# Performance work log

Hardware: AMD Instinct MI355X
Metric: run time of the kernel (lower is better)

The kernel has to match this reference:

```python
import jax, jax.numpy as jnp
import numpy as np

NUM_WORDS = 32768
MAX_CHARS = 20
NUM_CHARS = 128
EMB = 64
H = 128   # word_hidden_size (per direction)
C = 128   # context_vector_size


def setup_inputs() -> dict:
    key = jax.random.key(0)
    ks = jax.random.split(key, 16)
    s = 1.0 / np.sqrt(H)  # torch GRU default init scale
    u = lambda k, shape, sc: jax.random.uniform(k, shape, jnp.float32, -sc, sc)
    inp = {
        'padded_char_tensor': jax.random.randint(ks[0], (NUM_WORDS, MAX_CHARS), 0, NUM_CHARS),
        'sequence_lens': jax.random.randint(ks[1], (NUM_WORDS,), 1, MAX_CHARS + 1),
        'emb': jax.random.normal(ks[2], (NUM_CHARS, EMB), jnp.float32),
        # forward-direction GRU params (torch layout: gates r,z,n stacked)
        'Wih_f': u(ks[3], (3 * H, EMB), s),
        'Whh_f': u(ks[4], (3 * H, H), s),
        'bih_f': u(ks[5], (3 * H,), s),
        'bhh_f': u(ks[6], (3 * H,), s),
        # backward-direction GRU params
        'Wih_b': u(ks[7], (3 * H, EMB), s),
        'Whh_b': u(ks[8], (3 * H, H), s),
        'bih_b': u(ks[9], (3 * H,), s),
        'bhh_b': u(ks[10], (3 * H,), s),
        # word_projection Linear(2H -> C)
        'Wp': u(ks[11], (C, 2 * H), 1.0 / np.sqrt(2 * H)),
        'bp': u(ks[12], (C,), 1.0 / np.sqrt(2 * H)),
        # word context vector [C, 1]
        'ctx': u(ks[13], (C, 1), 0.1),
    }
    return inp


def _gru_dir(x_proj, Whh, bhh):
    # x_proj: [B, T, 3H] precomputed input projection; scan over T
    Hn = Whh.shape[1]
    def step(h, xt):
        hp = h @ Whh.T + bhh
        r = jax.nn.sigmoid(xt[:, :Hn] + hp[:, :Hn])
        z = jax.nn.sigmoid(xt[:, Hn:2 * Hn] + hp[:, Hn:2 * Hn])
        n = jnp.tanh(xt[:, 2 * Hn:] + r * hp[:, 2 * Hn:])
        h = (1.0 - z) * n + z * h
        return h, h
    h0 = jnp.zeros((x_proj.shape[0], Hn), x_proj.dtype)
    _, ys = jax.lax.scan(step, h0, x_proj.transpose(1, 0, 2))
    return ys.transpose(1, 0, 2)  # [B, T, H]


def _rev_within(x, lens):
    # reverse each sequence within its valid length (packed-sequence semantics)
    T = x.shape[1]
    t = jnp.arange(T)[None, :]
    idx = jnp.where(t < lens[:, None], lens[:, None] - 1 - t, t)
    return jnp.take_along_axis(x, idx[:, :, None], axis=1)


def _forward(chars, lens, emb, Wih_f, Whh_f, bih_f, bhh_f,
             Wih_b, Whh_b, bih_b, bhh_b, Wp, bp, ctx):
    x = emb[chars]  # [B, T, EMB]; dropout_p=0 -> identity
    mask = (jnp.arange(x.shape[1])[None, :] < lens[:, None])  # [B, T]
    out_f = _gru_dir(x @ Wih_f.T + bih_f, Whh_f, bhh_f)
    xb = _rev_within(x, lens)
    out_b = _gru_dir(xb @ Wih_b.T + bih_b, Whh_b, bhh_b)
    out_b = _rev_within(out_b, lens)
    # pad_packed_sequence zero-pads beyond each length
    out = jnp.concatenate([out_f, out_b], axis=-1) * mask[:, :, None]  # [B, T, 2H]
    proj = jnp.tanh(out @ Wp.T + bp)                # [B, T, C]
    scores = jnp.einsum('btc,c->bt', proj, ctx[:, 0])
    att = jax.nn.softmax(scores, axis=-1)           # softmax over char positions
    return jnp.einsum('bt,btd->bd', att, out)       # [B, 2H]


def reference(padded_char_tensor, sequence_lens, emb, Wih_f, Whh_f, bih_f, bhh_f,
              Wih_b, Whh_b, bih_b, bhh_b, Wp, bp, ctx):
    return _forward(padded_char_tensor, sequence_lens, emb, Wih_f, Whh_f, bih_f,
                    bhh_f, Wih_b, Whh_b, bih_b, bhh_b, Wp, bp, ctx)
```

## Files before the change

kernel.cpp:

```cpp
#include <hip/hip_runtime.h>
#include <hip/hip_bf16.h>
#include <stdint.h>


typedef unsigned short u16;
typedef float f32x4 __attribute__((ext_vector_type(4)));
typedef __bf16 bf16x8 __attribute__((ext_vector_type(8)));

#if __has_builtin(__builtin_amdgcn_exp2f)
#define EXP2F(x) __builtin_amdgcn_exp2f(x)
#else
#define EXP2F(x) exp2f(x)
#endif
#if __has_builtin(__builtin_amdgcn_rcpf)
#define RCPF(x) __builtin_amdgcn_rcpf(x)
#else
#define RCPF(x) (1.0f / (x))
#endif

#define LOG2E 1.4426950408889634f

__device__ __forceinline__ u16 f2b(float f) {
  uint32_t u = __builtin_bit_cast(uint32_t, f);
  u = u + 0x7FFFu + ((u >> 16) & 1u);
  return (u16)(u >> 16);
}
__device__ __forceinline__ float b2f(u16 s) {
  uint32_t u = ((uint32_t)s) << 16;
  return __builtin_bit_cast(float, u);
}
__device__ __forceinline__ float fast_tanh(float x) {
  return 1.0f - 2.0f * RCPF(EXP2F(2.0f * LOG2E * x) + 1.0f);
}
__device__ __forceinline__ uint32_t cvtpk(float a, float b) {
  uint32_t r;
  asm("v_cvt_pk_bf16_f32 %0, %1, %2" : "=v"(r) : "v"(a), "v"(b));
  return r;
}

__global__ void prep_kernel(
    const float* __restrict__ emb,
    const float* __restrict__ wih_f, const float* __restrict__ bih_f,
    const float* __restrict__ wih_b, const float* __restrict__ bih_b,
    const float* __restrict__ bhh_f, const float* __restrict__ bhh_b,
    const float* __restrict__ whh_f_in, const float* __restrict__ whh_b_in,
    const float* __restrict__ wp_in,
    float* __restrict__ xpf_f, float* __restrict__ xpf_b,
    u16* __restrict__ whhf, u16* __restrict__ whhb, u16* __restrict__ wpf) {
  int gid = blockIdx.x * 256 + threadIdx.x;
  if (blockIdx.x < 384) {
    int e = gid;
    int d = (e >= 49152) ? 1 : 0;
    int r = e - d * 49152;
    int j = r & 3;
    int e2 = r >> 2;
    int cls = e2 % 3;
    int e3 = e2 / 3;
    int grp = e3 & 3;
    int e4 = e3 >> 2;
    int wv = e4 & 7;
    int c = e4 >> 3;
    int row = cls * 128 + wv * 16 + grp * 4 + j;
    const float* wih = d ? wih_b : wih_f;
    const float* bih = d ? bih_b : bih_f;
    const float* bhh = d ? bhh_b : bhh_f;
    const float4* e4p = (const float4*)(emb + c * 64);
    const float4* w4p = (const float4*)(wih + row * 64);
    float s = 0.f;
#pragma unroll
    for (int q = 0; q < 16; q++) {
      float4 a = e4p[q], b = w4p[q];
      s += a.x * b.x + a.y * b.y + a.z * b.z + a.w * b.w;
    }
    s += bih[row];
    float scale;
    if (cls < 2) {
      s += bhh[row];
      scale = -LOG2E;
    } else {
      scale = 2.0f * LOG2E;
    }
    (d ? xpf_b : xpf_f)[r] = s * scale;
  } else if (blockIdx.x < 432) {
    int idx = gid - 384 * 256;
    int d = (idx >= 6144) ? 1 : 0;
    int r = idx - d * 6144;
    int lane = r & 63, kt = (r >> 6) & 3, nt = r >> 8;
    float scale = (nt < 16) ? -LOG2E : 2.0f * LOG2E;
    int n = nt * 16 + (lane & 15);
    int k0 = kt * 32 + (lane >> 4) * 8;
    const float* w = d ? whh_b_in : whh_f_in;
    u16* o = (d ? whhb : whhf) + r * 8;
    for (int j = 0; j < 8; j++) o[j] = f2b(w[n * 128 + k0 + j] * scale);
  } else {
    int idx = gid - 432 * 256;
    if (idx < 4096) {
      int lane = idx & 63, kt = (idx >> 6) & 7, nt = idx >> 9;
      int n = nt * 16 + (lane & 15);
      int k0 = kt * 32 + (lane >> 4) * 8;
      u16* o = wpf + idx * 8;
      for (int j = 0; j < 8; j++) o[j] = f2b(wp_in[n * 256 + k0 + j]);
    }
  }
}

__global__ void sort_zero(int* __restrict__ bins) {
  if (threadIdx.x < 32) bins[threadIdx.x] = 0;
}
__global__ void sort_hist(const int* __restrict__ lens, int* __restrict__ bins) {
  __shared__ int hcnt[32];
  int tid = threadIdx.x;
  if (tid < 32) hcnt[tid] = 0;
  __syncthreads();
  int gid = blockIdx.x * 256 + tid;
  int l = lens[gid] & 31;
  atomicAdd(&hcnt[l], 1);
  __syncthreads();
  if (tid < 32 && hcnt[tid]) atomicAdd(&bins[tid], hcnt[tid]);
}
__global__ void sort_scan(const int* __restrict__ bins, int* __restrict__ offsw,
                          const float* __restrict__ bp,
                          const float* __restrict__ ctx,
                          float* __restrict__ c0out) {
  if (threadIdx.x == 0 && blockIdx.x == 0) {
    int off = 0;
    for (int l = 0; l < 32; l++) {
      offsw[l] = off;
      off += bins[l];
    }
    float c0 = 0.f;
    for (int c = 0; c < 128; c++) c0 += fast_tanh(bp[c]) * ctx[c];
    *c0out = c0;
  }
}
__global__ void sort_scat(const int* __restrict__ lens, int* __restrict__ offsw,
                          int* __restrict__ perm) {
  __shared__ int lcnt[32];
  __shared__ int lbase[32];
  int tid = threadIdx.x;
  if (tid < 32) lcnt[tid] = 0;
  __syncthreads();
  int gid = blockIdx.x * 256 + tid;
  int l = lens[gid] & 31;
  int lr = atomicAdd(&lcnt[l], 1);
  __syncthreads();
  if (tid < 32) lbase[tid] = lcnt[tid] ? atomicAdd(&offsw[tid], lcnt[tid]) : 0;
  __syncthreads();
  perm[lbase[l] + lr] = gid;
}

__global__ __launch_bounds__(512, 4) void gru_kernel(
    const int* __restrict__ chars, const int* __restrict__ lens,
    const int* __restrict__ perm,
    const float* __restrict__ xpf_f, const float* __restrict__ xpf_b,
    const u16* __restrict__ whhf, const u16* __restrict__ whhb,
    const float* __restrict__ bhh_f, const float* __restrict__ bhh_b,
    u16* __restrict__ hf, u16* __restrict__ hb, int word_off, int nbd) {
  const int bid = blockIdx.x;
  const int dir = bid & 1;
  const int wg = nbd - 1 - (bid >> 1);
  const int tid = threadIdx.x;

  __shared__ int perm_s[32];
  __shared__ unsigned char lens_s[32];
  __shared__ int coff_s[640];
  __shared__ u16 h_s[2][4096];

  if (tid < 32) {
    int p = perm[word_off + wg * 32 + tid];
    perm_s[tid] = p;
    lens_s[tid] = (unsigned char)lens[p];
  }
  for (int i = tid; i < 2048; i += 512) ((uint32_t*)h_s)[i] = 0u;
  __syncthreads();
  for (int i = tid; i < 640; i += 512) {
    int w = i & 31, s = i >> 5;
    int L = lens_s[w];
    int t = dir ? ((s < L) ? (L - 1 - s) : s) : s;
    coff_s[s * 32 + w] = chars[perm_s[w] * 20 + t] * 384;
  }

  const float* xp = dir ? xpf_b : xpf_f;
  const u16* whh = dir ? whhb : whhf;
  const float* bhh = dir ? bhh_b : bhh_f;
  u16* hout = (dir ? hb : hf) + (size_t)wg * 32 * 2560;

  const int wv = tid >> 6, ln = tid & 63, word = ln & 15, grp = ln >> 4;
  const float* xpt = xp + (wv * 4 + grp) * 12;

  bf16x8 Wf[3][4];
#pragma unroll
  for (int cls = 0; cls < 3; cls++) {
    int nt = cls * 8 + wv;
#pragma unroll
    for (int kt = 0; kt < 4; kt++)
      Wf[cls][kt] = *(const bf16x8*)(whh + (((nt * 4 + kt) * 64 + ln) << 3));
  }
  float4 bhn = *(const float4*)(bhh + 256 + wv * 16 + grp * 4);
  bhn.x *= 2.0f * LOG2E; bhn.y *= 2.0f * LOG2E;
  bhn.z *= 2.0f * LOG2E; bhn.w *= 2.0f * LOG2E;

  __syncthreads();

  const int Lmax = lens_s[31];

  const int hw_off =
      (((wv >> 1) * 64) + (word | (((wv & 1) * 2 + (grp >> 1)) << 4))) * 16 +
      (grp & 1) * 8;
  const int sm = wv >> 2, skt = wv & 3;
  const int swl = sm * 16 + word;
  const int sLane = lens_s[swl];
  const int hs_off = (((sm * 4 + skt) * 64 + ln) << 4);
  u16* hsto = hout + (size_t)swl * 2560 + skt * 32 + (grp << 3);

  char* hsb = (char*)h_s;

  float h0[4] = {0.f, 0.f, 0.f, 0.f};
  float h1[4] = {0.f, 0.f, 0.f, 0.f};

#define GSTEP(S, PAR)                                                         \
  {                                                                           \
    int off0 = coff_s[(S) * 32 + word];                                       \
    int off1 = coff_s[(S) * 32 + 16 + word];                                  \
    f32x4 x00 = *(const f32x4*)(xpt + off0);                                  \
    f32x4 x01 = *(const f32x4*)(xpt + off0 + 4);                              \
    f32x4 x02 = *(const f32x4*)(xpt + off0 + 8);                              \
    f32x4 x10 = *(const f32x4*)(xpt + off1);                                  \
    f32x4 x11 = *(const f32x4*)(xpt + off1 + 4);                              \
    f32x4 x12 = *(const f32x4*)(xpt + off1 + 8);                              \
    f32x4 a0 = (f32x4){0.f, 0.f, 0.f, 0.f};                                   \
    f32x4 a1 = (f32x4){0.f, 0.f, 0.f, 0.f};                                   \
    f32x4 a2 = (f32x4){bhn.x, bhn.y, bhn.z, bhn.w};                           \
    f32x4 b0 = (f32x4){0.f, 0.f, 0.f, 0.f};                                   \
    f32x4 b1 = (f32x4){0.f, 0.f, 0.f, 0.f};                                   \
    f32x4 b2 = (f32x4){bhn.x, bhn.y, bhn.z, bhn.w};                           \
    _Pragma("unroll")                                                         \
    for (int kt = 0; kt < 4; kt++) {                                          \
      bf16x8 Hf0 =                                                            \
          *(const bf16x8*)(hsb + (PAR) * 8192 + ((kt * 64 + ln) << 4));       \
      a0 = __builtin_amdgcn_mfma_f32_16x16x32_bf16(Wf[0][kt], Hf0, a0, 0, 0, 0); \
      a1 = __builtin_amdgcn_mfma_f32_16x16x32_bf16(Wf[1][kt], Hf0, a1, 0, 0, 0); \
      a2 = __builtin_amdgcn_mfma_f32_16x16x32_bf16(Wf[2][kt], Hf0, a2, 0, 0, 0); \
    }                                                                         \
    _Pragma("unroll")                                                         \
    for (int kt = 0; kt < 4; kt++) {                                          \
      bf16x8 Hf1 = *(const bf16x8*)(hsb + (PAR) * 8192 +                      \
                                    (((4 + kt) * 64 + ln) << 4));             \
      b0 = __builtin_amdgcn_mfma_f32_16x16x32_bf16(Wf[0][kt], Hf1, b0, 0, 0, 0); \
      b1 = __builtin_amdgcn_mfma_f32_16x16x32_bf16(Wf[1][kt], Hf1, b1, 0, 0, 0); \
      b2 = __builtin_amdgcn_mfma_f32_16x16x32_bf16(Wf[2][kt], Hf1, b2, 0, 0, 0); \
    }                                                                         \
    _Pragma("unroll")                                                         \
    for (int r = 0; r < 4; r++) {                                             \
      float rr = RCPF(1.0f + EXP2F(x00[r] + a0[r]));                          \
      float zz = RCPF(1.0f + EXP2F(x01[r] + a1[r]));                          \
      float na = fmaf(rr, a2[r], x02[r]);                                     \
      float nn = fmaf(-2.0f, RCPF(EXP2F(na) + 1.0f), 1.0f);                   \
      h0[r] = fmaf(zz, h0[r] - nn, nn);                                       \
    }                                                                         \
    {                                                                         \
      uint2 pk = make_uint2(cvtpk(h0[0], h0[1]), cvtpk(h0[2], h0[3]));        \
      *(uint2*)(hsb + ((PAR) ^ 1) * 8192 + hw_off) = pk;                      \
    }                                                                         \
    _Pragma("unroll")                                                         \
    for (int r = 0; r < 4; r++) {                                             \
      float rr = RCPF(1.0f + EXP2F(x10[r] + b0[r]));                          \
      float zz = RCPF(1.0f + EXP2F(x11[r] + b1[r]));                          \
      float na = fmaf(rr, b2[r], x12[r]);                                     \
      float nn = fmaf(-2.0f, RCPF(EXP2F(na) + 1.0f), 1.0f);                   \
      h1[r] = fmaf(zz, h1[r] - nn, nn);                                       \
    }                                                                         \
    {                                                                         \
      uint2 pk = make_uint2(cvtpk(h1[0], h1[1]), cvtpk(h1[2], h1[3]));        \
      *(uint2*)(hsb + ((PAR) ^ 1) * 8192 + 4096 + hw_off) = pk;               \
    }                                                                         \
    __syncthreads();                                                          \
    if ((S) < sLane) {                                                        \
      int tdst = dir ? (sLane - 1 - (S)) : (S);                               \
      uint4 v = *(const uint4*)(hsb + ((PAR) ^ 1) * 8192 + hs_off);           \
      *(uint4*)(hsto + tdst * 128) = v;                                       \
    }                                                                         \
  }

  for (int s = 0; s < Lmax; s += 2) {
    GSTEP(s, 0);
    if (s + 1 < Lmax) GSTEP(s + 1, 1);
  }
#undef GSTEP
}

__global__ __launch_bounds__(256, 2) void attn_kernel(
    const u16* __restrict__ hf, const u16* __restrict__ hb,
    const u16* __restrict__ wpf,
    const float* __restrict__ bp, const float* __restrict__ ctx,
    const int* __restrict__ perm, const int* __restrict__ lens,
    const float* __restrict__ c0p,
    float* __restrict__ out, int word_off) {
  const int blk = gridDim.x - 1 - blockIdx.x;
  const int lw0 = blk * 16;

  __shared__ u16 ot_s[4096];
  __shared__ float part_s[4][16];
  __shared__ int perm_s[16];
  __shared__ unsigned char lens_s[16];

  const int tid = threadIdx.x;
  const int wv = tid >> 6, ln = tid & 63, col = ln & 15, grp = ln >> 4;
  const int sw = tid >> 4;
  const int seg = tid & 15;

  if (tid < 16) {
    int p = perm[word_off + lw0 + tid];
    perm_s[tid] = p;
    lens_s[tid] = (unsigned char)lens[p];
  }
  __syncthreads();
  const int Lmax = lens_s[15];
  const int Lw = lens_s[sw];

  float bpv[2], ctxv[2];
#pragma unroll
  for (int n = 0; n < 2; n++) {
    int nt = wv + n * 4;
    bpv[n] = bp[nt * 16 + col];
    ctxv[n] = ctx[nt * 16 + col];
  }

  float facc[16];
#pragma unroll
  for (int i = 0; i < 16; i++) facc[i] = 0.f;
  float mrun = -3.0e38f, drun = 0.f;

  const u16* srcbase =
      ((seg < 8) ? hf : hb) + (size_t)(lw0 + sw) * 2560 + (seg & 7) * 16;

  uint4 vn[2];
#pragma unroll
  for (int q = 0; q < 2; q++) vn[q] = *(const uint4*)(srcbase + q * 8);

  for (int t = 0; t < Lmax; t++) {
    uint4 v[2];
    v[0] = vn[0];
    v[1] = vn[1];

#pragma unroll
    for (int q = 0; q < 2; q++) {
      int idx = seg * 2 + q;
      int kt = idx >> 2;
      int lane_a = sw | ((idx & 3) << 4);
      *(uint4*)(ot_s + ((kt * 64 + lane_a) << 3)) = v[q];
    }
    if (t + 1 < Lmax) {
      const u16* src = srcbase + (t + 1) * 128;
#pragma unroll
      for (int q = 0; q < 2; q++) vn[q] = *(const uint4*)(src + q * 8);
    }
    __syncthreads();

    f32x4 acc[2];
#pragma unroll
    for (int n = 0; n < 2; n++) acc[n] = (f32x4){bpv[n], bpv[n], bpv[n], bpv[n]};

#pragma unroll
    for (int kt = 0; kt < 8; kt++) {
      bf16x8 Af = *(const bf16x8*)(ot_s + ((kt * 64 + ln) << 3));
#pragma unroll
      for (int n = 0; n < 2; n++) {
        int nt = wv + n * 4;
        bf16x8 Bf = *(const bf16x8*)(wpf + (((nt * 8 + kt) * 64 + ln) << 3));
        acc[n] = __builtin_amdgcn_mfma_f32_16x16x32_bf16(Af, Bf, acc[n], 0, 0, 0);
      }
    }

#pragma unroll
    for (int r = 0; r < 4; r++) {
      float p = fast_tanh(acc[0][r]) * ctxv[0] + fast_tanh(acc[1][r]) * ctxv[1];
      p += __shfl_xor(p, 1, 64);
      p += __shfl_xor(p, 2, 64);
      p += __shfl_xor(p, 4, 64);
      p += __shfl_xor(p, 8, 64);
      if (col == 0) part_s[wv][grp * 4 + r] = p;
    }
    __syncthreads();

    float sc = part_s[0][sw] + part_s[1][sw] + part_s[2][sw] + part_s[3][sw];

    if (t < Lw) {
      float mnew = fmaxf(mrun, sc);
      float scale = EXP2F(LOG2E * (mrun - mnew));
      float e = EXP2F(LOG2E * (sc - mnew));
      drun = drun * scale + e;
      mrun = mnew;
#pragma unroll
      for (int q = 0; q < 2; q++) {
        const u16* pv = (const u16*)&v[q];
#pragma unroll
        for (int j = 0; j < 8; j++)
          facc[q * 8 + j] = facc[q * 8 + j] * scale + e * b2f(pv[j]);
      }
    }
  }

  drun += (float)(20 - Lw) * EXP2F(LOG2E * (*c0p - mrun));

  float inv = RCPF(drun);
  float* dst = out + (size_t)perm_s[sw] * 256 + seg * 16;
#pragma unroll
  for (int i = 0; i < 4; i++) {
    float4 o = make_float4(facc[i * 4] * inv, facc[i * 4 + 1] * inv,
                           facc[i * 4 + 2] * inv, facc[i * 4 + 3] * inv);
    *(float4*)(dst + i * 4) = o;
  }
}

extern "C" void kernel_launch(void* const* d_in, const int* in_sizes, int n_in,
                              void* d_out, int out_size, void* d_ws, size_t ws_size,
                              hipStream_t stream) {
  const int* chars = (const int*)d_in[0];
  const int* lens = (const int*)d_in[1];
  const float* emb = (const float*)d_in[2];
  const float* wih_f = (const float*)d_in[3];
  const float* whh_f = (const float*)d_in[4];
  const float* bih_f = (const float*)d_in[5];
  const float* bhh_f = (const float*)d_in[6];
  const float* wih_b = (const float*)d_in[7];
  const float* whh_b = (const float*)d_in[8];
  const float* bih_b = (const float*)d_in[9];
  const float* bhh_b = (const float*)d_in[10];
  const float* wp = (const float*)d_in[11];
  const float* bp = (const float*)d_in[12];
  const float* ctx = (const float*)d_in[13];
  float* outp = (float*)d_out;

  uint8_t* ws = (uint8_t*)d_ws;
  float* xpf_f = (float*)(ws + 0);
  float* xpf_b = (float*)(ws + 196608);
  u16* whhf = (u16*)(ws + 393216);
  u16* whhb = (u16*)(ws + 491520);
  u16* wpf = (u16*)(ws + 589824);
  int* bins = (int*)(ws + 655360);
  int* offsw = (int*)(ws + 655488);
  float* c0p = (float*)(ws + 655616);
  int* permp = (int*)(ws + 655680);
  const size_t H_OFF = 1048576;

  prep_kernel<<<448, 256, 0, stream>>>(emb, wih_f, bih_f, wih_b, bih_b, bhh_f,
                                       bhh_b, whh_f, whh_b, wp, xpf_f, xpf_b,
                                       whhf, whhb, wpf);
  sort_zero<<<1, 64, 0, stream>>>(bins);
  sort_hist<<<128, 256, 0, stream>>>(lens, bins);
  sort_scan<<<1, 64, 0, stream>>>(bins, offsw, bp, ctx, c0p);
  sort_scat<<<128, 256, 0, stream>>>(lens, offsw, permp);

  const size_t per_word = 20 * 128 * 2 * 2;
  size_t avail = (ws_size > H_OFF) ? (ws_size - H_OFF) : 0;
  int maxw = (int)(avail / per_word) & ~63;
  if (maxw > 32768) maxw = 32768;
  if (maxw < 64) maxw = 64;

  for (int done = 0; done < 32768;) {
    int nw = (32768 - done < maxw) ? (32768 - done) : maxw;
    u16* hfp = (u16*)(ws + H_OFF);
    u16* hbp = hfp + (size_t)nw * 2560;
    int nbd = nw / 32;
    gru_kernel<<<2 * nbd, 512, 0, stream>>>(chars, lens, permp, xpf_f, xpf_b,
                                            whhf, whhb, bhh_f, bhh_b, hfp, hbp,
                                            done, nbd);
    attn_kernel<<<nw / 16, 256, 0, stream>>>(hfp, hbp, wpf, bp, ctx, permp,
                                             lens, c0p, outp, done);
    done += nw;
  }
}
```

Measured before the change: 278.3 us.

## Fuse backward GRU into attention kernel, run forward GRU separately

Splits the two-direction GRU kernel into a forward-only kernel and a new kernel that runs the backward GRU recurrence and the projection/attention pass together, 16 words per block. The backward hidden states stay in shared memory and feed the projection MFMAs directly instead of going through global memory, which halves the hidden-state workspace and removes one write/read round trip. In exchange the fused kernel does more serial work per step, processes 16 words instead of 32 per recurrence block, and holds more registers (projection weights as well as recurrent weights), which may reduce occupancy. The forward and backward recurrences no longer run concurrently within one launch.

```diff
diff --git a/kernel.cpp b/kernel.cpp
--- a/kernel.cpp
+++ b/kernel.cpp
@@ -149,16 +149,13 @@
   perm[lbase[l] + lr] = gid;
 }
 
-__global__ __launch_bounds__(512, 4) void gru_kernel(
+__global__ __launch_bounds__(512, 4) void gru_fwd(
     const int* __restrict__ chars, const int* __restrict__ lens,
     const int* __restrict__ perm,
-    const float* __restrict__ xpf_f, const float* __restrict__ xpf_b,
-    const u16* __restrict__ whhf, const u16* __restrict__ whhb,
-    const float* __restrict__ bhh_f, const float* __restrict__ bhh_b,
-    u16* __restrict__ hf, u16* __restrict__ hb, int word_off, int nbd) {
-  const int bid = blockIdx.x;
-  const int dir = bid & 1;
-  const int wg = nbd - 1 - (bid >> 1);
+    const float* __restrict__ xpf_f,
+    const u16* __restrict__ whhf, const float* __restrict__ bhh_f,
+    u16* __restrict__ hf, int word_off, int nbd) {
+  const int wg = nbd - 1 - blockIdx.x;
   const int tid = threadIdx.x;
 
   __shared__ int perm_s[32];
@@ -175,18 +172,13 @@
   __syncthreads();
   for (int i = tid; i < 640; i += 512) {
     int w = i & 31, s = i >> 5;
-    int L = lens_s[w];
-    int t = dir ? ((s < L) ? (L - 1 - s) : s) : s;
-    coff_s[s * 32 + w] = chars[perm_s[w] * 20 + t] * 384;
-  }
-
-  const float* xp = dir ? xpf_b : xpf_f;
-  const u16* whh = dir ? whhb : whhf;
-  const float* bhh = dir ? bhh_b : bhh_f;
-  u16* hout = (dir ? hb : hf) + (size_t)wg * 32 * 2560;
+    coff_s[s * 32 + w] = chars[perm_s[w] * 20 + s] * 384;
+  }
+
+  u16* hout = hf + (size_t)wg * 32 * 2560;
 
   const int wv = tid >> 6, ln = tid & 63, word = ln & 15, grp = ln >> 4;
-  const float* xpt = xp + (wv * 4 + grp) * 12;
+  const float* xpt = xpf_f + (wv * 4 + grp) * 12;
 
   bf16x8 Wf[3][4];
 #pragma unroll
@@ -194,9 +186,9 @@
     int nt = cls * 8 + wv;
 #pragma unroll
     for (int kt = 0; kt < 4; kt++)
-      Wf[cls][kt] = *(const bf16x8*)(whh + (((nt * 4 + kt) * 64 + ln) << 3));
-  }
-  float4 bhn = *(const float4*)(bhh + 256 + wv * 16 + grp * 4);
+      Wf[cls][kt] = *(const bf16x8*)(whhf + (((nt * 4 + kt) * 64 + ln) << 3));
+  }
+  float4 bhn = *(const float4*)(bhh_f + 256 + wv * 16 + grp * 4);
   bhn.x *= 2.0f * LOG2E; bhn.y *= 2.0f * LOG2E;
   bhn.z *= 2.0f * LOG2E; bhn.w *= 2.0f * LOG2E;
 
@@ -276,9 +268,8 @@
     }                                                                         \
     __syncthreads();                                                          \
     if ((S) < sLane) {                                                        \
-      int tdst = dir ? (sLane - 1 - (S)) : (S);                               \
       uint4 v = *(const uint4*)(hsb + ((PAR) ^ 1) * 8192 + hs_off);           \
-      *(uint4*)(hsto + tdst * 128) = v;                                       \
+      *(uint4*)(hsto + (S) * 128) = v;                                        \
     }                                                                         \
   }
 
@@ -289,128 +280,169 @@
 #undef GSTEP
 }
 
-__global__ __launch_bounds__(256, 2) void attn_kernel(
-    const u16* __restrict__ hf, const u16* __restrict__ hb,
-    const u16* __restrict__ wpf,
+__global__ __launch_bounds__(512, 2) void gru_bwd_attn(
+    const int* __restrict__ chars, const int* __restrict__ lens,
+    const int* __restrict__ perm,
+    const float* __restrict__ xpf_b,
+    const u16* __restrict__ whhb, const u16* __restrict__ wpf,
+    const float* __restrict__ bhh_b,
     const float* __restrict__ bp, const float* __restrict__ ctx,
-    const int* __restrict__ perm, const int* __restrict__ lens,
     const float* __restrict__ c0p,
-    float* __restrict__ out, int word_off) {
-  const int blk = gridDim.x - 1 - blockIdx.x;
+    const u16* __restrict__ hf, float* __restrict__ out,
+    int word_off, int nbA) {
+  const int blk = nbA - 1 - blockIdx.x;
   const int lw0 = blk * 16;
-
-  __shared__ u16 ot_s[4096];
-  __shared__ float part_s[4][16];
+  const int tid = threadIdx.x;
+
   __shared__ int perm_s[16];
   __shared__ unsigned char lens_s[16];
-
-  const int tid = threadIdx.x;
-  const int wv = tid >> 6, ln = tid & 63, col = ln & 15, grp = ln >> 4;
-  const int sw = tid >> 4;
-  const int seg = tid & 15;
+  __shared__ int coff_s[320];
+  __shared__ u16 h_s[2][2048];
+  __shared__ u16 ot_hf[2048];
+  __shared__ float part_s[8][16];
 
   if (tid < 16) {
     int p = perm[word_off + lw0 + tid];
     perm_s[tid] = p;
     lens_s[tid] = (unsigned char)lens[p];
   }
-  __syncthreads();
+  for (int i = tid; i < 1024; i += 512) ((uint32_t*)h_s)[i] = 0u;
+  __syncthreads();
+  for (int i = tid; i < 320; i += 512) {
+    int w = i & 15, s = i >> 4;
+    int L = lens_s[w];
+    int t = (s < L) ? (L - 1 - s) : s;
+    coff_s[s * 16 + w] = chars[perm_s[w] * 20 + t] * 384;
+  }
+
+  const int wv = tid >> 6, ln = tid & 63, word = ln & 15, grp = ln >> 4;
+  const float* xpt = xpf_b + (wv * 4 + grp) * 12;
+
+  bf16x8 Wf[3][4];
+#pragma unroll
+  for (int cls = 0; cls < 3; cls++) {
+    int nt = cls * 8 + wv;
+#pragma unroll
+    for (int kt = 0; kt < 4; kt++)
+      Wf[cls][kt] = *(const bf16x8*)(whhb + (((nt * 4 + kt) * 64 + ln) << 3));
+  }
+  bf16x8 Pf[8];
+#pragma unroll
+  for (int kt = 0; kt < 8; kt++)
+    Pf[kt] = *(const bf16x8*)(wpf + (((wv * 8 + kt) * 64 + ln) << 3));
+
+  float4 bhn = *(const float4*)(bhh_b + 256 + wv * 16 + grp * 4);
+  bhn.x *= 2.0f * LOG2E; bhn.y *= 2.0f * LOG2E;
+  bhn.z *= 2.0f * LOG2E; bhn.w *= 2.0f * LOG2E;
+  float4 bpv = *(const float4*)(bp + wv * 16 + grp * 4);
+  float4 ctxv = *(const float4*)(ctx + wv * 16 + grp * 4);
+  const float c0 = *c0p;
+
+  __syncthreads();
+
   const int Lmax = lens_s[15];
-  const int Lw = lens_s[sw];
-
-  float bpv[2], ctxv[2];
-#pragma unroll
-  for (int n = 0; n < 2; n++) {
-    int nt = wv + n * 4;
-    bpv[n] = bp[nt * 16 + col];
-    ctxv[n] = ctx[nt * 16 + col];
-  }
-
-  float facc[16];
-#pragma unroll
-  for (int i = 0; i < 16; i++) facc[i] = 0.f;
+  const int Lw = lens_s[word];
+
+  const int hw_off =
+      (((wv >> 1) * 64) + (word | (((wv & 1) * 2 + (grp >> 1)) << 4))) * 16 +
+      (grp & 1) * 8;
+  const int fr_lane = word | (grp << 4);
+  const int othf_off = ((wv * 64 + fr_lane) << 4);
+  const int hbr_off = (((wv - 4) * 64 + fr_lane) << 4);
+  const u16* hfb = hf + (size_t)(lw0 + word) * 2560 + (wv * 4 + grp) * 8;
+
+  char* hsb = (char*)h_s;
+  char* otb = (char*)ot_hf;
+
+  float hreg[4] = {0.f, 0.f, 0.f, 0.f};
+  float facc[8] = {0.f, 0.f, 0.f, 0.f, 0.f, 0.f, 0.f, 0.f};
   float mrun = -3.0e38f, drun = 0.f;
 
-  const u16* srcbase =
-      ((seg < 8) ? hf : hb) + (size_t)(lw0 + sw) * 2560 + (seg & 7) * 16;
-
-  uint4 vn[2];
-#pragma unroll
-  for (int q = 0; q < 2; q++) vn[q] = *(const uint4*)(srcbase + q * 8);
-
-  for (int t = 0; t < Lmax; t++) {
-    uint4 v[2];
-    v[0] = vn[0];
-    v[1] = vn[1];
-
-#pragma unroll
-    for (int q = 0; q < 2; q++) {
-      int idx = seg * 2 + q;
-      int kt = idx >> 2;
-      int lane_a = sw | ((idx & 3) << 4);
-      *(uint4*)(ot_s + ((kt * 64 + lane_a) << 3)) = v[q];
-    }
-    if (t + 1 < Lmax) {
-      const u16* src = srcbase + (t + 1) * 128;
-#pragma unroll
-      for (int q = 0; q < 2; q++) vn[q] = *(const uint4*)(src + q * 8);
-    }
+  for (int s = 0; s < Lmax; s++) {
+    const int PAR = (s & 1) * 4096;
+    const int NPAR = PAR ^ 4096;
+
+    uint4 hfc = make_uint4(0u, 0u, 0u, 0u);
+    if (wv < 4) {
+      int tl = (s < Lw) ? (Lw - 1 - s) : 0;
+      hfc = *(const uint4*)(hfb + tl * 128);
+    }
+
+    int off = coff_s[s * 16 + word];
+    f32x4 x0 = *(const f32x4*)(xpt + off);
+    f32x4 x1 = *(const f32x4*)(xpt + off + 4);
+    f32x4 x2 = *(const f32x4*)(xpt + off + 8);
+    f32x4 a0 = (f32x4){0.f, 0.f, 0.f, 0.f};
+    f32x4 a1 = (f32x4){0.f, 0.f, 0.f, 0.f};
+    f32x4 a2 = (f32x4){bhn.x, bhn.y, bhn.z, bhn.w};
+#pragma unroll
+    for (int kt = 0; kt < 4; kt++) {
+      bf16x8 Hf = *(const bf16x8*)(hsb + PAR + ((kt * 64 + ln) << 4));
+      a0 = __builtin_amdgcn_mfma_f32_16x16x32_bf16(Wf[0][kt], Hf, a0, 0, 0, 0);
+      a1 = __builtin_amdgcn_mfma_f32_16x16x32_bf16(Wf[1][kt], Hf, a1, 0, 0, 0);
+      a2 = __builtin_amdgcn_mfma_f32_16x16x32_bf16(Wf[2][kt], Hf, a2, 0, 0, 0);
+    }
+#pragma unroll
+    for (int r = 0; r < 4; r++) {
+      float rr = RCPF(1.0f + EXP2F(x0[r] + a0[r]));
+      float zz = RCPF(1.0f + EXP2F(x1[r] + a1[r]));
+      float na = fmaf(rr, a2[r], x2[r]);
+      float nn = fmaf(-2.0f, RCPF(EXP2F(na) + 1.0f), 1.0f);
+      hreg[r] = fmaf(zz, hreg[r] - nn, nn);
+    }
+    {
+      uint2 pk = make_uint2(cvtpk(hreg[0], hreg[1]), cvtpk(hreg[2], hreg[3]));
+      *(uint2*)(hsb + NPAR + hw_off) = pk;
+    }
+    if (wv < 4) *(uint4*)(otb + othf_off) = hfc;
     __syncthreads();
 
-    f32x4 acc[2];
-#pragma unroll
-    for (int n = 0; n < 2; n++) acc[n] = (f32x4){bpv[n], bpv[n], bpv[n], bpv[n]};
-
-#pragma unroll
-    for (int kt = 0; kt < 8; kt++) {
-      bf16x8 Af = *(const bf16x8*)(ot_s + ((kt * 64 + ln) << 3));
-#pragma unroll
-      for (int n = 0; n < 2; n++) {
-        int nt = wv + n * 4;
-        bf16x8 Bf = *(const bf16x8*)(wpf + (((nt * 8 + kt) * 64 + ln) << 3));
-        acc[n] = __builtin_amdgcn_mfma_f32_16x16x32_bf16(Af, Bf, acc[n], 0, 0, 0);
-      }
-    }
-
-#pragma unroll
-    for (int r = 0; r < 4; r++) {
-      float p = fast_tanh(acc[0][r]) * ctxv[0] + fast_tanh(acc[1][r]) * ctxv[1];
-      p += __shfl_xor(p, 1, 64);
-      p += __shfl_xor(p, 2, 64);
-      p += __shfl_xor(p, 4, 64);
-      p += __shfl_xor(p, 8, 64);
-      if (col == 0) part_s[wv][grp * 4 + r] = p;
-    }
+    f32x4 pa = (f32x4){bpv.x, bpv.y, bpv.z, bpv.w};
+#pragma unroll
+    for (int kt = 0; kt < 4; kt++) {
+      bf16x8 Bf = *(const bf16x8*)(otb + ((kt * 64 + ln) << 4));
+      pa = __builtin_amdgcn_mfma_f32_16x16x32_bf16(Pf[kt], Bf, pa, 0, 0, 0);
+    }
+#pragma unroll
+    for (int kt = 4; kt < 8; kt++) {
+      bf16x8 Bf = *(const bf16x8*)(hsb + NPAR + (((kt - 4) * 64 + ln) << 4));
+      pa = __builtin_amdgcn_mfma_f32_16x16x32_bf16(Pf[kt], Bf, pa, 0, 0, 0);
+    }
+    uint4 hbv = make_uint4(0u, 0u, 0u, 0u);
+    if (wv >= 4) hbv = *(const uint4*)(hsb + NPAR + hbr_off);
+
+    float p = fast_tanh(pa[0]) * ctxv.x + fast_tanh(pa[1]) * ctxv.y +
+              fast_tanh(pa[2]) * ctxv.z + fast_tanh(pa[3]) * ctxv.w;
+    p += __shfl_xor(p, 16, 64);
+    p += __shfl_xor(p, 32, 64);
+    if (ln < 16) part_s[wv][ln] = p;
     __syncthreads();
 
-    float sc = part_s[0][sw] + part_s[1][sw] + part_s[2][sw] + part_s[3][sw];
-
-    if (t < Lw) {
+    if (s < Lw) {
+      float sc = part_s[0][word] + part_s[1][word] + part_s[2][word] +
+                 part_s[3][word] + part_s[4][word] + part_s[5][word] +
+                 part_s[6][word] + part_s[7][word];
       float mnew = fmaxf(mrun, sc);
       float scale = EXP2F(LOG2E * (mrun - mnew));
       float e = EXP2F(LOG2E * (sc - mnew));
       drun = drun * scale + e;
       mrun = mnew;
-#pragma unroll
-      for (int q = 0; q < 2; q++) {
-        const u16* pv = (const u16*)&v[q];
-#pragma unroll
-        for (int j = 0; j < 8; j++)
-          facc[q * 8 + j] = facc[q * 8 + j] * scale + e * b2f(pv[j]);
-      }
-    }
-  }
-
-  drun += (float)(20 - Lw) * EXP2F(LOG2E * (*c0p - mrun));
-
+      const u16* pv = (wv < 4) ? (const u16*)&hfc : (const u16*)&hbv;
+#pragma unroll
+      for (int j = 0; j < 8; j++)
+        facc[j] = facc[j] * scale + e * b2f(pv[j]);
+    }
+  }
+
+  drun += (float)(20 - Lw) * EXP2F(LOG2E * (c0 - mrun));
   float inv = RCPF(drun);
-  float* dst = out + (size_t)perm_s[sw] * 256 + seg * 16;
-#pragma unroll
-  for (int i = 0; i < 4; i++) {
-    float4 o = make_float4(facc[i * 4] * inv, facc[i * 4 + 1] * inv,
-                           facc[i * 4 + 2] * inv, facc[i * 4 + 3] * inv);
-    *(float4*)(dst + i * 4) = o;
-  }
+  float* dst = out + (size_t)perm_s[word] * 256 + (wv * 4 + grp) * 8;
+  float4 o0 = make_float4(facc[0] * inv, facc[1] * inv, facc[2] * inv,
+                          facc[3] * inv);
+  float4 o1 = make_float4(facc[4] * inv, facc[5] * inv, facc[6] * inv,
+                          facc[7] * inv);
+  *(float4*)(dst) = o0;
+  *(float4*)(dst + 4) = o1;
 }
 
 extern "C" void kernel_launch(void* const* d_in, const int* in_sizes, int n_in,
@@ -452,7 +484,7 @@
   sort_scan<<<1, 64, 0, stream>>>(bins, offsw, bp, ctx, c0p);
   sort_scat<<<128, 256, 0, stream>>>(lens, offsw, permp);
 
-  const size_t per_word = 20 * 128 * 2 * 2;
+  const size_t per_word = 20 * 128 * 2;
   size_t avail = (ws_size > H_OFF) ? (ws_size - H_OFF) : 0;
   int maxw = (int)(avail / per_word) & ~63;
   if (maxw > 32768) maxw = 32768;
@@ -461,13 +493,13 @@
   for (int done = 0; done < 32768;) {
     int nw = (32768 - done < maxw) ? (32768 - done) : maxw;
     u16* hfp = (u16*)(ws + H_OFF);
-    u16* hbp = hfp + (size_t)nw * 2560;
     int nbd = nw / 32;
-    gru_kernel<<<2 * nbd, 512, 0, stream>>>(chars, lens, permp, xpf_f, xpf_b,
-                                            whhf, whhb, bhh_f, bhh_b, hfp, hbp,
-                                            done, nbd);
-    attn_kernel<<<nw / 16, 256, 0, stream>>>(hfp, hbp, wpf, bp, ctx, permp,
-                                             lens, c0p, outp, done);
+    int nbA = nw / 16;
+    gru_fwd<<<nbd, 512, 0, stream>>>(chars, lens, permp, xpf_f, whhf, bhh_f,
+                                     hfp, done, nbd);
+    gru_bwd_attn<<<nbA, 512, 0, stream>>>(chars, lens, permp, xpf_b, whhb,
+                                          wpf, bhh_b, bp, ctx, c0p, hfp, outp,
+                                          done, nbA);
     done += nw;
   }
 }
```

Result: slower. 285.2 us (+2.5%).
